# Optimization experiments

Measured on AMD Instinct MI355X. Metric: run time of the kernel, lower is better.

The kernel has to match this reference:

```python
import jax, jax.numpy as jnp
import numpy as np

HEADS = 8
GS = 16
C = 512
E = 512
SCALE = (E / HEADS) ** -0.5
PNAMES = ['sa_qkv_w','sa_qkv_b','sa_pa_w','sa_pa_b','sa_ln1_g','sa_ln1_b','sa_f1_w','sa_f1_b','sa_f2_w','sa_f2_b','sa_ln2_g','sa_ln2_b','sa_c1_w','sa_c1_b','sa_c2_w','sa_c2_b','sa_bn_g','sa_bn_b','ca_q_w','ca_q_b','ca_k_w','ca_k_b','ca_v_w','ca_v_b','ca_pa_w','ca_pa_b','p_q_w','p_q_b','p_k_w','p_k_b','p_v_w','p_v_b','p_pa_w','p_pa_b','p_ln_g','p_ln_b','p_lin_w','p_lin_b']


def _ln(x, g, b, eps=1e-5):
    m = x.mean(-1, keepdims=True)
    v = jnp.var(x, axis=-1, keepdims=True)
    return (x - m) / jnp.sqrt(v + eps) * g + b


def _conv1x1(x, w, b):
    return jnp.einsum('bchw,oc->bohw', x, w) + b[None, :, None, None]


def _up_ac(x, out=GS):
    # bilinear upsample, align_corners=True (nn.UpsamplingBilinear2d)
    H = x.shape[2]
    pos = jnp.arange(out) * (H - 1) / (out - 1)
    lo = jnp.floor(pos).astype(jnp.int32)
    hi = jnp.minimum(lo + 1, H - 1)
    w = (pos - lo).astype(x.dtype)
    xr = x[:, :, lo, :] * (1 - w)[None, None, :, None] + x[:, :, hi, :] * w[None, None, :, None]
    return xr[:, :, :, lo] * (1 - w) + xr[:, :, :, hi] * w


def _asri(x, p):
    # Sequence_ASRI: GAP tokens -> attention over the batch axis -> pixel-shuffle back
    B = x.shape[0]; ch = E // HEADS
    gap = x.mean((2, 3))                                             # [B,C]
    qkv = (gap @ p['sa_qkv_w'].T + p['sa_qkv_b']).reshape(B, 4, ch, HEADS).transpose(1, 3, 0, 2)  # [4,H,B,ch]
    q, k, v, skip = qkv[0], qkv[1], qkv[2], qkv[3]
    attn = jax.nn.softmax(jnp.einsum('hbc,hdc->hbd', q, k) * SCALE, -1)  # [H,B,B]
    o = jnp.einsum('hbd,hdc->hbc', attn, v)
    merge = lambda t: t.transpose(1, 2, 0).reshape(B, E)             # 'head b c -> b (c head)'
    a = merge(o) @ p['sa_pa_w'].T + p['sa_pa_b'] + merge(skip)
    h = jax.nn.relu(_ln(a, p['sa_ln1_g'], p['sa_ln1_b']) @ p['sa_f1_w'].T + p['sa_f1_b'])
    a = h @ p['sa_f2_w'].T + p['sa_f2_b'] + a
    s = _ln(a, p['sa_ln2_g'], p['sa_ln2_b']) @ p['sa_c1_w'].T + p['sa_c1_b']  # [B,C*16]
    s = _up_ac(s.reshape(B, C, 4, 4))                                 # pixel shuffle p1=p2=4 then bilinear to 16x16
    s = _conv1x1(s, p['sa_c2_w'], p['sa_c2_b'])
    # BatchNorm2d in eval mode (running_mean=0, running_var=1, eps=1e-5)
    s = s / np.float32(np.sqrt(1.0 + 1e-5)) * p['sa_bn_g'][None, :, None, None] + p['sa_bn_b'][None, :, None, None]
    return x + jax.nn.relu(s)


def _sscm(x1, x2, p):
    # Sequence_SSCM: GAP-token q/k over batch axis, full spatial v
    B = x1.shape[0]; ch = E // HEADS
    q = (x1.mean((2, 3)) @ p['ca_q_w'].T + p['ca_q_b']).reshape(B, ch, HEADS).transpose(2, 0, 1)  # [H,B,ch]
    k = (x2.mean((2, 3)) @ p['ca_k_w'].T + p['ca_k_b']).reshape(B, ch, HEADS).transpose(2, 0, 1)
    v = _conv1x1(x2, p['ca_v_w'], p['ca_v_b']).reshape(B, ch, HEADS, GS, GS).transpose(2, 0, 1, 3, 4).reshape(HEADS, B, ch * GS * GS)
    attn = jax.nn.softmax(jnp.einsum('hbc,hdc->hbd', q, k) * SCALE, -1)  # [H,B,B]
    o = jnp.einsum('hbd,hdm->hbm', attn, v)
    o = o.reshape(HEADS, B, ch, GS, GS).transpose(1, 2, 0, 3, 4).reshape(B, E, GS, GS)
    return jax.nn.relu(_conv1x1(o, p['ca_pa_w'], p['ca_pa_b']))


def _pixel(x1, x2, p):
    # Pixel_SSCM: pixel-wise cross-batch attention (no scale -- matches source)
    B = x1.shape[0]; ch = E // HEADS; N = GS * GS
    split = lambda t: t.reshape(B, ch, HEADS, N).transpose(2, 0, 3, 1)   # 'b (c head) h w -> head b (h w) c'
    q = split(_conv1x1(x1, p['p_q_w'], p['p_q_b']))                      # [H,B,N,ch]
    k = split(_conv1x1(x2, p['p_k_w'], p['p_k_b']))
    v = split(_conv1x1(x2, p['p_v_w'], p['p_v_b'])).reshape(HEADS, B * N, ch)
    attn = jax.nn.softmax(jnp.einsum('hbnc,hqmc->hbqnm', q, k), -1)      # [H,B,B,N,N]
    attn = attn.transpose(1, 0, 3, 2, 4).reshape(B, HEADS, N, B * N)     # 'head b q h w -> b head h (q w)'
    o = jnp.einsum('bhnm,hmc->bhnc', attn, v)
    o = o.transpose(0, 3, 1, 2).reshape(B, E, GS, GS)                    # 'b head (h w) c -> b (c head) h w'
    o = _conv1x1(o, p['p_pa_w'], p['p_pa_b']) + x1
    t = o.reshape(B, C, N).transpose(0, 2, 1)                            # [B,N,C]
    t = jax.nn.relu(_ln(t, p['p_ln_g'], p['p_ln_b']) @ p['p_lin_w'].T + p['p_lin_b'])
    return t.transpose(0, 2, 1).reshape(B, C, GS, GS)


def _hrlm(p, xs, xq):
    sa_s = _asri(xs, p)
    sa_q = _asri(xq, p)
    ca_s = _sscm(sa_s, sa_q, p)
    ca_q = _sscm(sa_q, sa_s, p)
    return _pixel(sa_s, ca_q, p), _pixel(sa_q, ca_s, p)


def setup_inputs():
    key = jax.random.key(0)
    ks = iter(jax.random.split(key, 64))
    w = lambda *s: (jax.random.normal(next(ks), s) * 0.02).astype(jnp.float32)
    z = lambda n: jnp.zeros((n,), jnp.float32)
    o = lambda n: jnp.ones((n,), jnp.float32)
    return dict(
        fea_support=jax.random.normal(next(ks), (8, C, GS, GS), jnp.float32),
        fea_query=jax.random.normal(next(ks), (8, C, GS, GS), jnp.float32),
        sa_qkv_w=w(4 * E, C), sa_qkv_b=z(4 * E),
        sa_pa_w=w(E, E), sa_pa_b=z(E),
        sa_ln1_g=o(E), sa_ln1_b=z(E),
        sa_f1_w=w(E, E), sa_f1_b=z(E), sa_f2_w=w(E, E), sa_f2_b=z(E),
        sa_ln2_g=o(E), sa_ln2_b=z(E),
        sa_c1_w=w(C * 16, E), sa_c1_b=z(C * 16),
        sa_c2_w=w(C, E), sa_c2_b=z(C),
        sa_bn_g=o(C), sa_bn_b=z(C),
        ca_q_w=w(E, C), ca_q_b=z(E), ca_k_w=w(E, C), ca_k_b=z(E),
        ca_v_w=w(E, C), ca_v_b=z(E), ca_pa_w=w(C, E), ca_pa_b=z(C),
        p_q_w=w(E, C), p_q_b=z(E), p_k_w=w(E, C), p_k_b=z(E),
        p_v_w=w(E, C), p_v_b=z(E), p_pa_w=w(C, E), p_pa_b=z(C),
        p_ln_g=o(C), p_ln_b=z(C), p_lin_w=w(C, C), p_lin_b=z(C),
    )


def reference(fea_support, fea_query, sa_qkv_w, sa_qkv_b, sa_pa_w, sa_pa_b, sa_ln1_g, sa_ln1_b, sa_f1_w, sa_f1_b, sa_f2_w, sa_f2_b, sa_ln2_g, sa_ln2_b, sa_c1_w, sa_c1_b, sa_c2_w, sa_c2_b, sa_bn_g, sa_bn_b, ca_q_w, ca_q_b, ca_k_w, ca_k_b, ca_v_w, ca_v_b, ca_pa_w, ca_pa_b, p_q_w, p_q_b, p_k_w, p_k_b, p_v_w, p_v_b, p_pa_w, p_pa_b, p_ln_g, p_ln_b, p_lin_w, p_lin_b):
    p = dict(zip(PNAMES, (sa_qkv_w, sa_qkv_b, sa_pa_w, sa_pa_b, sa_ln1_g, sa_ln1_b, sa_f1_w, sa_f1_b, sa_f2_w, sa_f2_b, sa_ln2_g, sa_ln2_b, sa_c1_w, sa_c1_b, sa_c2_w, sa_c2_b, sa_bn_g, sa_bn_b, ca_q_w, ca_q_b, ca_k_w, ca_k_b, ca_v_w, ca_v_b, ca_pa_w, ca_pa_b, p_q_w, p_q_b, p_k_w, p_k_b, p_v_w, p_v_b, p_pa_w, p_pa_b, p_ln_g, p_ln_b, p_lin_w, p_lin_b)))
    return _hrlm(p, fea_support, fea_query)
```

## Files before the change

kernel.cpp:

```cpp
#include <hip/hip_runtime.h>
#include <cmath>

#define IMG 131072
#define BIGF 1048576
#define PLANE 1048576

#define CF_RELU  1
#define CF_RES   2
#define CF_BN    4
#define CF_SPLIT 8

typedef __attribute__((ext_vector_type(8))) short short8;
typedef __attribute__((ext_vector_type(4))) short short4v;
typedef __attribute__((ext_vector_type(4))) float f32x4;

__device__ __forceinline__ float wave_sum(float v){
    #pragma unroll
    for (int off = 32; off; off >>= 1) v += __shfl_xor(v, off);
    return v;
}

__device__ __forceinline__ unsigned short bf16_rn(float x){
    union { float f; unsigned u; } v; v.f = x;
    unsigned r = v.u + 0x7FFF + ((v.u >> 16) & 1);
    return (unsigned short)(r >> 16);
}
__device__ __forceinline__ float bf16_to_f(unsigned short h){
    union { float f; unsigned u; } v; v.u = ((unsigned)h) << 16;
    return v.f;
}

struct GapJobs  { const float* x[2]; float* o[2]; };
struct G8Job    { const float* in; const float* W; const float* bias; const float* add; float* out; };
struct G8Jobs   { G8Job j[4]; };
struct AAJobs   { const float* qkv[2]; float* om[2]; };
struct LnJobs   { const float* in[2]; float* out[2]; };
struct UpJobs   { const float* in[2]; float* out[2]; };
struct SAJobs   { const float* q8[2]; const float* k8[2]; float* aw[2]; };
struct SPJobs   { const float* aw[2]; const float* v[2]; float* out[2]; };
struct ZJobs    { float* p[2]; };
struct ConvJob  { const float* X; const float* W; const float* B; const float* R;
                  const float* bng; const float* bnb; float* O; int flags; };
struct ConvJobs { ConvJob j[6]; };
struct PixJob   { const unsigned short* Q; const unsigned short* K; const unsigned short* V; float* O; };
struct PixJobs  { PixJob j[2]; };

__global__ __launch_bounds__(64) void k_gap(GapJobs jo){
    const int br = blockIdx.y;
    const int bc = blockIdx.x;
    const int lane = threadIdx.x;
    const float* p = jo.x[br] + (size_t)bc * 256;
    float s = p[lane] + p[lane + 64] + p[lane + 128] + p[lane + 192];
    s = wave_sum(s);
    if (lane == 0) jo.o[br][bc] = s * (1.0f / 256.0f);
}

__global__ __launch_bounds__(64) void k_gemm8(G8Jobs jo, int add_off, int add_stride, int O, int relu){
    const G8Job j = jo.j[blockIdx.y];
    const int o = blockIdx.x;
    const int lane = threadIdx.x;
    const float* wr = j.W + (size_t)o * 512;
    float acc[8] = {0,0,0,0,0,0,0,0};
    #pragma unroll
    for (int i = 0; i < 8; i++){
        float w = wr[lane + 64*i];
        #pragma unroll
        for (int b = 0; b < 8; b++) acc[b] += w * j.in[b*512 + lane + 64*i];
    }
    #pragma unroll
    for (int b = 0; b < 8; b++) acc[b] = wave_sum(acc[b]);
    if (lane < 8){
        float v = acc[0];
        #pragma unroll
        for (int b = 1; b < 8; b++) if (lane == b) v = acc[b];
        v += j.bias[o];
        if (j.add) v += j.add[lane*add_stride + add_off + o];
        if (relu) v = fmaxf(v, 0.f);
        j.out[(size_t)lane * O + o] = v;
    }
}

__global__ __launch_bounds__(64) void k_asri_attn(AAJobs jo){
    const int br = blockIdx.y;
    const float* qkv = jo.qkv[br];
    const int h = blockIdx.x >> 3, b = blockIdx.x & 7, c = threadIdx.x;
    const int ci = c*8 + h;
    float qc = qkv[b*2048 + ci];
    float s[8];
    #pragma unroll
    for (int d = 0; d < 8; d++){
        float p = qc * qkv[d*2048 + 512 + ci];
        p = wave_sum(p);
        s[d] = p * 0.125f;
    }
    float m = s[0];
    #pragma unroll
    for (int d = 1; d < 8; d++) m = fmaxf(m, s[d]);
    float sum = 0.f;
    #pragma unroll
    for (int d = 0; d < 8; d++){ s[d] = __expf(s[d]-m); sum += s[d]; }
    float r = 1.f / sum;
    float oc = 0.f;
    #pragma unroll
    for (int d = 0; d < 8; d++) oc += s[d]*r * qkv[d*2048 + 1024 + ci];
    jo.om[br][b*512 + ci] = oc;
}

__global__ __launch_bounds__(64) void k_ln8(LnJobs jo,
    const float* __restrict__ g, const float* __restrict__ be)
{
    const int br = blockIdx.y;
    const int b = blockIdx.x, lane = threadIdx.x;
    const float* in = jo.in[br];
    float v[8]; float s = 0.f;
    #pragma unroll
    for (int i = 0; i < 8; i++){ v[i] = in[b*512 + lane + 64*i]; s += v[i]; }
    s = wave_sum(s);
    float mean = s * (1.f/512.f);
    float q = 0.f;
    #pragma unroll
    for (int i = 0; i < 8; i++){ float d = v[i]-mean; q += d*d; }
    q = wave_sum(q);
    float rstd = rsqrtf(q*(1.f/512.f) + 1e-5f);
    #pragma unroll
    for (int i = 0; i < 8; i++){
        int c = lane + 64*i;
        jo.out[br][b*512 + c] = (v[i]-mean)*rstd*g[c] + be[c];
    }
}

__global__ __launch_bounds__(256) void k_up(UpJobs jo){
    const int br = blockIdx.y;
    const int idx = blockIdx.x*256 + threadIdx.x;
    const int x = idx & 15, y = (idx >> 4) & 15, bc = idx >> 8;
    float px = (float)(x*3) / 15.0f, py = (float)(y*3) / 15.0f;
    int lx = (int)px, ly = (int)py;
    float wx = px - lx, wy = py - ly;
    int hx = min(lx+1, 3), hy = min(ly+1, 3);
    const float* p = jo.in[br] + (size_t)bc * 16;
    float v00 = p[ly*4+lx], v01 = p[ly*4+hx], v10 = p[hy*4+lx], v11 = p[hy*4+hx];
    float a0 = v00*(1.f-wy) + v10*wy;
    float a1 = v01*(1.f-wy) + v11*wy;
    jo.out[br][idx] = a0*(1.f-wx) + a1*wx;
}

__global__ __launch_bounds__(256) void k_zero(ZJobs jo){
    jo.p[blockIdx.y][(size_t)blockIdx.x*256 + threadIdx.x] = 0.f;
}

#define LDK 40
__device__ __forceinline__ void convm_body(
    const float* __restrict__ Xb, const float* __restrict__ W,
    const float* __restrict__ bias, const float* __restrict__ resb,
    const float* __restrict__ bng, const float* __restrict__ bnb, float bninv,
    float* __restrict__ outb, int flags, int o0, int n0, unsigned short* lds)
{
    const int tid512 = threadIdx.x;
    const int g   = tid512 >> 8;
    const int tid = tid512 & 255;
    unsigned short* sAh = lds + g*10240;
    unsigned short* sAl = sAh + 2560;
    unsigned short* sBh = sAl + 2560;
    unsigned short* sBl = sBh + 2560;
    const int wv = tid >> 6, lane = tid & 63;
    const int quad = lane >> 4, l16 = lane & 15;
    const int wo = (wv >> 1) * 32, wn = (wv & 1) * 32;
    const int so  = tid >> 2, sk8 = (tid & 3) * 8;
    const int sp  = tid & 15, sn  = (tid >> 4) * 4;

    const float* wrow = W + (size_t)(o0 + so)*512 + g*256 + sk8;
    const float* xrow = Xb + (size_t)(g*256 + 2*sp)*256 + n0 + sn;

    f32x4 acc[2][2] = {};
    float4 a0 = *(const float4*)(wrow);
    float4 a1 = *(const float4*)(wrow + 4);
    float4 x0 = *(const float4*)(xrow);
    float4 x1 = *(const float4*)(xrow + 256);

    for (int k0 = 0; k0 < 256; k0 += 32){
        __syncthreads();
        {
            float wa[8] = {a0.x,a0.y,a0.z,a0.w,a1.x,a1.y,a1.z,a1.w};
            #pragma unroll
            for (int j = 0; j < 4; j++){
                unsigned short h0 = bf16_rn(wa[2*j]);
                unsigned short h1 = bf16_rn(wa[2*j+1]);
                unsigned short g0 = bf16_rn(wa[2*j]   - bf16_to_f(h0));
                unsigned short g1 = bf16_rn(wa[2*j+1] - bf16_to_f(h1));
                *(unsigned*)&sAh[so*LDK + sk8 + 2*j] = (unsigned)h0 | ((unsigned)h1 << 16);
                *(unsigned*)&sAl[so*LDK + sk8 + 2*j] = (unsigned)g0 | ((unsigned)g1 << 16);
            }
            float xe[4] = {x0.x,x0.y,x0.z,x0.w};
            float xo[4] = {x1.x,x1.y,x1.z,x1.w};
            #pragma unroll
            for (int j = 0; j < 4; j++){
                unsigned short h0 = bf16_rn(xe[j]);
                unsigned short h1 = bf16_rn(xo[j]);
                unsigned short g0 = bf16_rn(xe[j] - bf16_to_f(h0));
                unsigned short g1 = bf16_rn(xo[j] - bf16_to_f(h1));
                *(unsigned*)&sBh[(sn+j)*LDK + 2*sp] = (unsigned)h0 | ((unsigned)h1 << 16);
                *(unsigned*)&sBl[(sn+j)*LDK + 2*sp] = (unsigned)g0 | ((unsigned)g1 << 16);
            }
        }
        __syncthreads();
        if (k0 + 32 < 256){
            a0 = *(const float4*)(wrow + k0 + 32);
            a1 = *(const float4*)(wrow + k0 + 36);
            x0 = *(const float4*)(xrow + (size_t)(k0+32)*256);
            x1 = *(const float4*)(xrow + (size_t)(k0+32)*256 + 256);
        }
        short8 ah[2], al[2], bh[2], bl[2];
        #pragma unroll
        for (int t = 0; t < 2; t++){
            int ai = (wo + 16*t + l16)*LDK + quad*8;
            ah[t] = *(const short8*)&sAh[ai];
            al[t] = *(const short8*)&sAl[ai];
            int bi = (wn + 16*t + l16)*LDK + quad*8;
            bh[t] = *(const short8*)&sBh[bi];
            bl[t] = *(const short8*)&sBl[bi];
        }
        #pragma unroll
        for (int mt = 0; mt < 2; mt++){
            #pragma unroll
            for (int nt = 0; nt < 2; nt++){
                acc[mt][nt] = __builtin_amdgcn_mfma_f32_16x16x32_bf16(ah[mt], bh[nt], acc[mt][nt], 0, 0, 0);
                acc[mt][nt] = __builtin_amdgcn_mfma_f32_16x16x32_bf16(ah[mt], bl[nt], acc[mt][nt], 0, 0, 0);
                acc[mt][nt] = __builtin_amdgcn_mfma_f32_16x16x32_bf16(al[mt], bh[nt], acc[mt][nt], 0, 0, 0);
            }
        }
    }
    __syncthreads();
    float* red = (float*)lds;
    if (g == 1){
        float* r = red + tid*20;
        #pragma unroll
        for (int mt = 0; mt < 2; mt++)
            #pragma unroll
            for (int nt = 0; nt < 2; nt++)
                *(f32x4*)(r + (mt*2+nt)*4) = acc[mt][nt];
    }
    __syncthreads();
    if (g == 0){
        float* r = red + tid*20;
        #pragma unroll
        for (int mt = 0; mt < 2; mt++)
            #pragma unroll
            for (int nt = 0; nt < 2; nt++){
                f32x4 o4 = *(const f32x4*)(r + (mt*2+nt)*4);
                acc[mt][nt] += o4;
            }
        #pragma unroll
        for (int mt = 0; mt < 2; mt++){
            #pragma unroll
            for (int nt = 0; nt < 2; nt++){
                const int n  = n0 + wn + 16*nt + l16;
                const int ob = o0 + wo + 16*mt + quad*4;
                #pragma unroll
                for (int rr = 0; rr < 4; rr++){
                    const int o = ob + rr;
                    float v = acc[mt][nt][rr] + bias[o];
                    if (flags & CF_BN)   v = v*(bninv*bng[o]) + bnb[o];
                    if (flags & CF_RELU) v = fmaxf(v, 0.f);
                    if (flags & CF_RES)  v += resb[(size_t)o*256 + n];
                    if (flags & CF_SPLIT){
                        unsigned short hi = bf16_rn(v);
                        unsigned short lo = bf16_rn(v - bf16_to_f(hi));
                        unsigned short* oh = (unsigned short*)outb;
                        oh[(size_t)o*256 + n] = hi;
                        oh[PLANE + (size_t)o*256 + n] = lo;
                    } else {
                        outb[(size_t)o*256 + n] = v;
                    }
                }
            }
        }
    }
}

__global__ __launch_bounds__(512) void k_convm(ConvJobs jo, float bninv)
{
    __shared__ unsigned short lds[20480];
    const int z = blockIdx.z;
    const ConvJob j = jo.j[z >> 3];
    const int b = z & 7;
    float* ob = (j.flags & CF_SPLIT) ? j.O + (size_t)b*(IMG/2) : j.O + (size_t)b*IMG;
    convm_body(j.X + (size_t)b*IMG, j.W, j.B, j.R ? j.R + (size_t)b*IMG : nullptr,
               j.bng, j.bnb, bninv, ob, j.flags,
               blockIdx.y*64, blockIdx.x*64, lds);
}

__global__ __launch_bounds__(64) void k_sscm_attn(SAJobs jo)
{
    const int br = blockIdx.y;
    const int h = blockIdx.x >> 3, b = blockIdx.x & 7, c = threadIdx.x;
    const int ci = c*8 + h;
    float qc = jo.q8[br][b*512 + ci];
    float s[8];
    #pragma unroll
    for (int d = 0; d < 8; d++){
        float p = qc * jo.k8[br][d*512 + ci];
        p = wave_sum(p);
        s[d] = p * 0.125f;
    }
    float m = s[0];
    #pragma unroll
    for (int d = 1; d < 8; d++) m = fmaxf(m, s[d]);
    float sum = 0.f;
    #pragma unroll
    for (int d = 0; d < 8; d++){ s[d] = __expf(s[d]-m); sum += s[d]; }
    float r = 1.f/sum;
    if (c < 8){
        float v = s[0];
        #pragma unroll
        for (int d = 1; d < 8; d++) if (c == d) v = s[d];
        jo.aw[br][blockIdx.x*8 + c] = v*r;
    }
}

__global__ __launch_bounds__(256) void k_sscm_apply(SPJobs jo)
{
    const int br = blockIdx.y;
    const int idx = blockIdx.x*256 + threadIdx.x;
    const int pix = idx & 255, e = (idx >> 8) & 511, b = idx >> 17;
    const int h = e & 7;
    const float* aw = jo.aw[br] + (h*8 + b)*8;
    const float* v = jo.v[br];
    float acc = 0.f;
    #pragma unroll
    for (int d = 0; d < 8; d++) acc += aw[d] * v[(size_t)d*IMG + (size_t)e*256 + pix];
    jo.out[br][idx] = acc;
}

__global__ __launch_bounds__(256) void k_pixel_mfma(PixJobs jo)
{
    __shared__ char smem[61440];
    unsigned short* sQh = (unsigned short*)smem;
    unsigned short* sQl = sQh + 2*64*40;
    unsigned short* sKh = sQl + 2*64*40;
    unsigned short* sKl = sKh + 2*128*40;
    unsigned short* sP  = (unsigned short*)smem;
    unsigned short* sVh = sP  + 4*64*40;
    unsigned short* sVl = sVh + 4*64*40;

    const int br = blockIdx.y >> 3, b = blockIdx.y & 7;
    const PixJob J = jo.j[br];
    const int nt = blockIdx.x & 3, d = blockIdx.x >> 2;
    const int h = blockIdx.z;
    const int tid = threadIdx.x;
    const int wv = tid >> 6, lane = tid & 63;
    const int quad = lane >> 4, l16 = lane & 15;
    const int n0 = nt * 64;

    const unsigned short* Qh = J.Q + (size_t)b * 131072;
    const unsigned short* Ql = Qh + PLANE;
    const unsigned short* Kh = J.K + (size_t)d * 131072;
    const unsigned short* Kl = Kh + PLANE;
    const unsigned short* Vh = J.V + (size_t)d * 131072;
    const unsigned short* Vl = Vh + PLANE;

    {
        const int q = tid & 63, c0 = tid >> 6;
        #pragma unroll
        for (int r = 0; r < 16; r++){
            int c = c0 + 4*r;
            int src = (c*8+h)*256 + n0 + q;
            int idx = (c>>5)*2560 + q*40 + (c&31);
            sQh[idx] = Qh[src];
            sQl[idx] = Ql[src];
        }
    }
    __syncthreads();

    short8 bqh[2], bql[2];
    #pragma unroll
    for (int ks = 0; ks < 2; ks++){
        int idx = ks*2560 + (wv*16 + l16)*40 + quad*8;
        bqh[ks] = *(const short8*)&sQh[idx];
        bql[ks] = *(const short8*)&sQl[idx];
    }

    f32x4 S[16] = {};
    #pragma unroll
    for (int hm = 0; hm < 2; hm++){
        __syncthreads();
        {
            const int mloc = tid & 127, cb0 = tid >> 7;
            #pragma unroll
            for (int p = 0; p < 4; p++){
                int cb = cb0 + 2*p;
                short8 hi8, lo8;
                #pragma unroll
                for (int j = 0; j < 8; j++){
                    int src = ((cb*8+j)*8+h)*256 + hm*128 + mloc;
                    hi8[j] = (short)Kh[src];
                    lo8[j] = (short)Kl[src];
                }
                int idx = (cb>>2)*5120 + mloc*40 + (cb&3)*8;
                *(short8*)&sKh[idx] = hi8;
                *(short8*)&sKl[idx] = lo8;
            }
        }
        __syncthreads();
        #pragma unroll
        for (int mtl = 0; mtl < 8; mtl++){
            #pragma unroll
            for (int ks = 0; ks < 2; ks++){
                int idx = ks*5120 + (mtl*16 + l16)*40 + quad*8;
                short8 ah = *(const short8*)&sKh[idx];
                short8 al = *(const short8*)&sKl[idx];
                S[hm*8+mtl] = __builtin_amdgcn_mfma_f32_16x16x32_bf16(ah, bqh[ks], S[hm*8+mtl], 0, 0, 0);
                S[hm*8+mtl] = __builtin_amdgcn_mfma_f32_16x16x32_bf16(ah, bql[ks], S[hm*8+mtl], 0, 0, 0);
                S[hm*8+mtl] = __builtin_amdgcn_mfma_f32_16x16x32_bf16(al, bqh[ks], S[hm*8+mtl], 0, 0, 0);
            }
        }
    }

    {
        float mx = -3.4e38f;
        #pragma unroll
        for (int t = 0; t < 16; t++)
            #pragma unroll
            for (int r = 0; r < 4; r++) mx = fmaxf(mx, S[t][r]);
        mx = fmaxf(mx, __shfl_xor(mx, 16));
        mx = fmaxf(mx, __shfl_xor(mx, 32));
        float sum = 0.f;
        #pragma unroll
        for (int t = 0; t < 16; t++)
            #pragma unroll
            for (int r = 0; r < 4; r++){ S[t][r] = __expf(S[t][r]-mx); sum += S[t][r]; }
        sum += __shfl_xor(sum, 16);
        sum += __shfl_xor(sum, 32);
        float rr = 1.f/sum;
        #pragma unroll
        for (int t = 0; t < 16; t++)
            #pragma unroll
            for (int r = 0; r < 4; r++) S[t][r] *= rr;
    }

    f32x4 oac[4] = {};
    #pragma unroll
    for (int hm = 0; hm < 2; hm++){
        __syncthreads();
        #pragma unroll
        for (int mtl = 0; mtl < 8; mtl++){
            short4v p4;
            #pragma unroll
            for (int r = 0; r < 4; r++) p4[r] = (short)bf16_rn(S[hm*8+mtl][r]);
            int idx = (mtl>>1)*2560 + (wv*16 + l16)*40 + 16*(mtl&1) + quad*4;
            *(short4v*)&sP[idx] = p4;
        }
        {
            const int mp = tid & 63, c0 = tid >> 6;
            #pragma unroll
            for (int p = 0; p < 16; p++){
                int c = c0 + 4*p;
                int src = (c*8+h)*256 + hm*128 + 2*mp;
                int idx = (mp>>4)*2560 + c*40 + ((2*mp)&31);
                *(unsigned*)&sVh[idx] = *(const unsigned*)&Vh[src];
                *(unsigned*)&sVl[idx] = *(const unsigned*)&Vl[src];
            }
        }
        __syncthreads();
        #pragma unroll
        for (int ks = 0; ks < 4; ks++){
            int pidx = ks*2560 + (wv*16 + l16)*40 + quad*8;
            short8 bp = *(const short8*)&sP[pidx];
            #pragma unroll
            for (int ct = 0; ct < 4; ct++){
                int vidx = ks*2560 + (ct*16 + l16)*40 + quad*8;
                short8 vh = *(const short8*)&sVh[vidx];
                short8 vl = *(const short8*)&sVl[vidx];
                oac[ct] = __builtin_amdgcn_mfma_f32_16x16x32_bf16(vh, bp, oac[ct], 0, 0, 0);
                oac[ct] = __builtin_amdgcn_mfma_f32_16x16x32_bf16(vl, bp, oac[ct], 0, 0, 0);
            }
        }
    }

    {
        float* Ob = J.O + (size_t)b * IMG;
        const int q = n0 + wv*16 + l16;
        #pragma unroll
        for (int ct = 0; ct < 4; ct++){
            #pragma unroll
            for (int r = 0; r < 4; r++){
                int c = ct*16 + quad*4 + r;
                unsafeAtomicAdd(&Ob[(size_t)(c*8+h)*256 + q], oac[ct][r]);
            }
        }
    }
}

__global__ __launch_bounds__(64) void k_ln_pix(LnJobs jo,
    const float* __restrict__ g, const float* __restrict__ be)
{
    const int br = blockIdx.y;
    const int bn = blockIdx.x;
    const int b = bn >> 8, n = bn & 255;
    const int lane = threadIdx.x;
    const float* p = jo.in[br] + (size_t)b*IMG + n;
    float v[8]; float s = 0.f;
    #pragma unroll
    for (int i = 0; i < 8; i++){ v[i] = p[(size_t)(lane + 64*i)*256]; s += v[i]; }
    s = wave_sum(s);
    float mean = s * (1.f/512.f);
    float q = 0.f;
    #pragma unroll
    for (int i = 0; i < 8; i++){ float d = v[i]-mean; q += d*d; }
    q = wave_sum(q);
    float rstd = rsqrtf(q*(1.f/512.f) + 1e-5f);
    #pragma unroll
    for (int i = 0; i < 8; i++){
        int c = lane + 64*i;
        jo.out[br][(size_t)b*IMG + (size_t)c*256 + n] = (v[i]-mean)*rstd*g[c] + be[c];
    }
}

extern "C" void kernel_launch(void* const* d_in, const int* in_sizes, int n_in,
                              void* d_out, int out_size, void* d_ws, size_t ws_size,
                              hipStream_t stream)
{
    const float* xs    = (const float*)d_in[0];
    const float* xq    = (const float*)d_in[1];
    const float* qkvw  = (const float*)d_in[2];  const float* qkvb = (const float*)d_in[3];
    const float* paw   = (const float*)d_in[4];  const float* pab  = (const float*)d_in[5];
    const float* ln1g  = (const float*)d_in[6];  const float* ln1b = (const float*)d_in[7];
    const float* f1w   = (const float*)d_in[8];  const float* f1b  = (const float*)d_in[9];
    const float* f2w   = (const float*)d_in[10]; const float* f2b  = (const float*)d_in[11];
    const float* ln2g  = (const float*)d_in[12]; const float* ln2b = (const float*)d_in[13];
    const float* c1w   = (const float*)d_in[14]; const float* c1b  = (const float*)d_in[15];
    const float* c2w   = (const float*)d_in[16]; const float* c2b  = (const float*)d_in[17];
    const float* bng   = (const float*)d_in[18]; const float* bnb  = (const float*)d_in[19];
    const float* caqw  = (const float*)d_in[20]; const float* caqb = (const float*)d_in[21];
    const float* cakw  = (const float*)d_in[22]; const float* cakb = (const float*)d_in[23];
    const float* cavw  = (const float*)d_in[24]; const float* cavb = (const float*)d_in[25];
    const float* capw  = (const float*)d_in[26]; const float* capb = (const float*)d_in[27];
    const float* pqw   = (const float*)d_in[28]; const float* pqb  = (const float*)d_in[29];
    const float* pkw   = (const float*)d_in[30]; const float* pkb  = (const float*)d_in[31];
    const float* pvw   = (const float*)d_in[32]; const float* pvb  = (const float*)d_in[33];
    const float* ppw   = (const float*)d_in[34]; const float* ppb  = (const float*)d_in[35];
    const float* plng  = (const float*)d_in[36]; const float* plnb = (const float*)d_in[37];
    const float* plinw = (const float*)d_in[38]; const float* plinb= (const float*)d_in[39];

    const size_t SMF = 262144;
    float* ws = (float*)d_ws;
    float* smb = ws;
    float* B[12];
    for (int i = 0; i < 12; i++) B[i] = ws + SMF + (size_t)i*BIGF;
    float* sa_s = B[0]; float* sa_q = B[1];
    float* ca_s = B[2]; float* ca_q = B[3];
    const bool paired_pixel = ws_size >= (SMF + 12*(size_t)BIGF)*sizeof(float) + 1024;

    auto SM = [&](int br){ return smb + (size_t)br*131072; };
    auto GAP=[&](int br){ return SM(br); };            auto QKV=[&](int br){ return SM(br)+4096; };
    auto OM =[&](int br){ return SM(br)+20480; };      auto AA =[&](int br){ return SM(br)+24576; };
    auto HB =[&](int br){ return SM(br)+28672; };      auto A2 =[&](int br){ return SM(br)+32768; };
    auto LNB=[&](int br){ return SM(br)+36864; };      auto S8 =[&](int br){ return SM(br)+40960; };
    auto ATW=[&](int br){ return SM(br)+106496; };     auto Q8 =[&](int br){ return SM(br)+107008; };
    auto K8 =[&](int br){ return SM(br)+111104; };

    const float bninv = 1.0f / sqrtf(1.0f + 1e-5f);
    float* out0 = (float*)d_out;
    float* out1 = out0 + (size_t)BIGF;

    {
        GapJobs gj = {{xs, xq}, {GAP(0), GAP(1)}};
        k_gap<<<dim3(4096,2), 64, 0, stream>>>(gj);
        G8Jobs qj = {{{GAP(0), qkvw, qkvb, nullptr, QKV(0)}, {GAP(1), qkvw, qkvb, nullptr, QKV(1)}}};
        k_gemm8<<<dim3(2048,2), 64, 0, stream>>>(qj, 0, 0, 2048, 0);
        AAJobs aj = {{QKV(0), QKV(1)}, {OM(0), OM(1)}};
        k_asri_attn<<<dim3(64,2), 64, 0, stream>>>(aj);
        G8Jobs pj = {{{OM(0), paw, pab, QKV(0), AA(0)}, {OM(1), paw, pab, QKV(1), AA(1)}}};
        k_gemm8<<<dim3(512,2), 64, 0, stream>>>(pj, 1536, 2048, 512, 0);
        LnJobs l1 = {{AA(0), AA(1)}, {LNB(0), LNB(1)}};
        k_ln8<<<dim3(8,2), 64, 0, stream>>>(l1, ln1g, ln1b);
        G8Jobs fj = {{{LNB(0), f1w, f1b, nullptr, HB(0)}, {LNB(1), f1w, f1b, nullptr, HB(1)}}};
        k_gemm8<<<dim3(512,2), 64, 0, stream>>>(fj, 0, 0, 512, 1);
        G8Jobs f2j = {{{HB(0), f2w, f2b, AA(0), A2(0)}, {HB(1), f2w, f2b, AA(1), A2(1)}}};
        k_gemm8<<<dim3(512,2), 64, 0, stream>>>(f2j, 0, 512, 512, 0);
        LnJobs l2 = {{A2(0), A2(1)}, {LNB(0), LNB(1)}};
        k_ln8<<<dim3(8,2), 64, 0, stream>>>(l2, ln2g, ln2b);
        G8Jobs cj = {{{LNB(0), c1w, c1b, nullptr, S8(0)}, {LNB(1), c1w, c1b, nullptr, S8(1)}}};
        k_gemm8<<<dim3(8192,2), 64, 0, stream>>>(cj, 0, 0, 8192, 0);
        UpJobs uj = {{S8(0), S8(1)}, {B[4], B[5]}};
        k_up<<<dim3(4096,2), 256, 0, stream>>>(uj);
        ConvJobs c2j = {};
        c2j.j[0] = {B[4], c2w, c2b, xs, bng, bnb, sa_s, CF_BN|CF_RELU|CF_RES};
        c2j.j[1] = {B[5], c2w, c2b, xq, bng, bnb, sa_q, CF_BN|CF_RELU|CF_RES};
        k_convm<<<dim3(4,8,16), 512, 0, stream>>>(c2j, bninv);
    }

    {
        GapJobs gj = {{sa_s, sa_q}, {GAP(0), GAP(1)}};
        k_gap<<<dim3(4096,2), 64, 0, stream>>>(gj);
        G8Jobs qj = {{{GAP(0), caqw, caqb, nullptr, Q8(0)},
                      {GAP(1), cakw, cakb, nullptr, K8(0)},
                      {GAP(1), caqw, caqb, nullptr, Q8(1)},
                      {GAP(0), cakw, cakb, nullptr, K8(1)}}};
        k_gemm8<<<dim3(512,4), 64, 0, stream>>>(qj, 0, 0, 512, 0);
        SAJobs sj = {{Q8(0), Q8(1)}, {K8(0), K8(1)}, {ATW(0), ATW(1)}};
        k_sscm_attn<<<dim3(64,2), 64, 0, stream>>>(sj);
        ConvJobs vj = {};
        vj.j[0] = {sa_q, cavw, cavb, nullptr, nullptr, nullptr, B[4], 0};
        vj.j[1] = {sa_s, cavw, cavb, nullptr, nullptr, nullptr, B[5], 0};
        k_convm<<<dim3(4,8,16), 512, 0, stream>>>(vj, 1.f);
        SPJobs pj = {{ATW(0), ATW(1)}, {B[4], B[5]}, {B[6], B[7]}};
        k_sscm_apply<<<dim3(4096,2), 256, 0, stream>>>(pj);
        ConvJobs aj = {};
        aj.j[0] = {B[6], capw, capb, nullptr, nullptr, nullptr, ca_s, CF_RELU};
        aj.j[1] = {B[7], capw, capb, nullptr, nullptr, nullptr, ca_q, CF_RELU};
        k_convm<<<dim3(4,8,16), 512, 0, stream>>>(aj, 1.f);
    }

    if (paired_pixel){
        ConvJobs qkvj = {};
        qkvj.j[0] = {sa_s, pqw, pqb, nullptr, nullptr, nullptr, B[4],  CF_SPLIT};
        qkvj.j[1] = {ca_q, pkw, pkb, nullptr, nullptr, nullptr, B[5],  CF_SPLIT};
        qkvj.j[2] = {ca_q, pvw, pvb, nullptr, nullptr, nullptr, B[6],  CF_SPLIT};
        qkvj.j[3] = {sa_q, pqw, pqb, nullptr, nullptr, nullptr, B[8],  CF_SPLIT};
        qkvj.j[4] = {ca_s, pkw, pkb, nullptr, nullptr, nullptr, B[9],  CF_SPLIT};
        qkvj.j[5] = {ca_s, pvw, pvb, nullptr, nullptr, nullptr, B[10], CF_SPLIT};
        k_convm<<<dim3(4,8,48), 512, 0, stream>>>(qkvj, 1.f);
        ZJobs zj = {{B[7], B[11]}};
        k_zero<<<dim3(4096,2), 256, 0, stream>>>(zj);
        PixJobs pxj = {{{(const unsigned short*)B[4], (const unsigned short*)B[5], (const unsigned short*)B[6], B[7]},
                        {(const unsigned short*)B[8], (const unsigned short*)B[9], (const unsigned short*)B[10], B[11]}}};
        k_pixel_mfma<<<dim3(32,16,8), 256, 0, stream>>>(pxj);
        ConvJobs ppj = {};
        ppj.j[0] = {B[7],  ppw, ppb, sa_s, nullptr, nullptr, out0, CF_RES};
        ppj.j[1] = {B[11], ppw, ppb, sa_q, nullptr, nullptr, out1, CF_RES};
        k_convm<<<dim3(4,8,16), 512, 0, stream>>>(ppj, 1.f);
        LnJobs lj = {{out0, out1}, {B[4], B[8]}};
        k_ln_pix<<<dim3(2048,2), 64, 0, stream>>>(lj, plng, plnb);
        ConvJobs lnj = {};
        lnj.j[0] = {B[4], plinw, plinb, nullptr, nullptr, nullptr, out0, CF_RELU};
        lnj.j[1] = {B[8], plinw, plinb, nullptr, nullptr, nullptr, out1, CF_RELU};
        k_convm<<<dim3(4,8,16), 512, 0, stream>>>(lnj, 1.f);
    } else {
        auto pixel1 = [&](const float* x1, const float* x2, float* out){
            ConvJobs qkvj = {};
            qkvj.j[0] = {x1, pqw, pqb, nullptr, nullptr, nullptr, B[4], CF_SPLIT};
            qkvj.j[1] = {x2, pkw, pkb, nullptr, nullptr, nullptr, B[5], CF_SPLIT};
            qkvj.j[2] = {x2, pvw, pvb, nullptr, nullptr, nullptr, B[6], CF_SPLIT};
            k_convm<<<dim3(4,8,24), 512, 0, stream>>>(qkvj, 1.f);
            ZJobs zj = {{B[7], B[7]}};
            k_zero<<<dim3(4096,1), 256, 0, stream>>>(zj);
            PixJobs pxj = {{{(const unsigned short*)B[4], (const unsigned short*)B[5], (const unsigned short*)B[6], B[7]},
                            {(const unsigned short*)B[4], (const unsigned short*)B[5], (const unsigned short*)B[6], B[7]}}};
            k_pixel_mfma<<<dim3(32,8,8), 256, 0, stream>>>(pxj);
            ConvJobs ppj = {};
            ppj.j[0] = {B[7], ppw, ppb, x1, nullptr, nullptr, out, CF_RES};
            k_convm<<<dim3(4,8,8), 512, 0, stream>>>(ppj, 1.f);
            LnJobs lj = {{out, out}, {B[4], B[4]}};
            k_ln_pix<<<dim3(2048,1), 64, 0, stream>>>(lj, plng, plnb);
            ConvJobs lnj = {};
            lnj.j[0] = {B[4], plinw, plinb, nullptr, nullptr, nullptr, out, CF_RELU};
            k_convm<<<dim3(4,8,8), 512, 0, stream>>>(lnj, 1.f);
        };
        pixel1(sa_s, ca_q, out0);
        pixel1(sa_q, ca_s, out1);
    }

    (void)in_sizes; (void)n_in; (void)out_size;
}
```

Baseline: 579.3 us.

## Interleave hi/lo bf16 split planes and transpose Q/K for vectorized pixel-attention loads

The QKV 1x1 conv now packs the hi and lo bf16 halves of each value into one 32-bit word instead of writing two separate planes. For Q and K it also writes a transposed, head-grouped layout (pixel-major, then head, then channel). The pixel attention kernel can then stage Q and K tiles with 16-byte vector loads and split hi/lo with byte permutes, replacing strided per-element 2-byte gathers. The transposed epilogue stores are scattered with a 2 KB stride, which may cost write efficiency in the conv kernel.

```diff
diff --git a/kernel.cpp b/kernel.cpp
--- a/kernel.cpp
+++ b/kernel.cpp
@@ -3,12 +3,12 @@
 
 #define IMG 131072
 #define BIGF 1048576
-#define PLANE 1048576
 
 #define CF_RELU  1
 #define CF_RES   2
 #define CF_BN    4
 #define CF_SPLIT 8
+#define CF_TRANS 16
 
 typedef __attribute__((ext_vector_type(8))) short short8;
 typedef __attribute__((ext_vector_type(4))) short short4v;
@@ -28,6 +28,12 @@
 __device__ __forceinline__ float bf16_to_f(unsigned short h){
     union { float f; unsigned u; } v; v.u = ((unsigned)h) << 16;
     return v.f;
+}
+__device__ __forceinline__ unsigned pk_hi(unsigned a, unsigned b){
+    return __builtin_amdgcn_perm(b, a, 0x05040100u);
+}
+__device__ __forceinline__ unsigned pk_lo(unsigned a, unsigned b){
+    return __builtin_amdgcn_perm(b, a, 0x07060302u);
 }
 
 struct GapJobs  { const float* x[2]; float* o[2]; };
@@ -42,7 +48,7 @@
 struct ConvJob  { const float* X; const float* W; const float* B; const float* R;
                   const float* bng; const float* bnb; float* O; int flags; };
 struct ConvJobs { ConvJob j[6]; };
-struct PixJob   { const unsigned short* Q; const unsigned short* K; const unsigned short* V; float* O; };
+struct PixJob   { const unsigned* Q; const unsigned* K; const unsigned* V; float* O; };
 struct PixJobs  { PixJob j[2]; };
 
 __global__ __launch_bounds__(64) void k_gap(GapJobs jo){
@@ -265,9 +271,10 @@
                     if (flags & CF_SPLIT){
                         unsigned short hi = bf16_rn(v);
                         unsigned short lo = bf16_rn(v - bf16_to_f(hi));
-                        unsigned short* oh = (unsigned short*)outb;
-                        oh[(size_t)o*256 + n] = hi;
-                        oh[PLANE + (size_t)o*256 + n] = lo;
+                        unsigned pk = (unsigned)hi | ((unsigned)lo << 16);
+                        unsigned* op = (unsigned*)outb;
+                        if (flags & CF_TRANS) op[(size_t)n*512 + (o&7)*64 + (o>>3)] = pk;
+                        else                  op[(size_t)o*256 + n] = pk;
                     } else {
                         outb[(size_t)o*256 + n] = v;
                     }
@@ -283,9 +290,8 @@
     const int z = blockIdx.z;
     const ConvJob j = jo.j[z >> 3];
     const int b = z & 7;
-    float* ob = (j.flags & CF_SPLIT) ? j.O + (size_t)b*(IMG/2) : j.O + (size_t)b*IMG;
     convm_body(j.X + (size_t)b*IMG, j.W, j.B, j.R ? j.R + (size_t)b*IMG : nullptr,
-               j.bng, j.bnb, bninv, ob, j.flags,
+               j.bng, j.bnb, bninv, j.O + (size_t)b*IMG, j.flags,
                blockIdx.y*64, blockIdx.x*64, lds);
 }
 
@@ -351,23 +357,24 @@
     const int quad = lane >> 4, l16 = lane & 15;
     const int n0 = nt * 64;
 
-    const unsigned short* Qh = J.Q + (size_t)b * 131072;
-    const unsigned short* Ql = Qh + PLANE;
-    const unsigned short* Kh = J.K + (size_t)d * 131072;
-    const unsigned short* Kl = Kh + PLANE;
-    const unsigned short* Vh = J.V + (size_t)d * 131072;
-    const unsigned short* Vl = Vh + PLANE;
-
     {
-        const int q = tid & 63, c0 = tid >> 6;
-        #pragma unroll
-        for (int r = 0; r < 16; r++){
-            int c = c0 + 4*r;
-            int src = (c*8+h)*256 + n0 + q;
-            int idx = (c>>5)*2560 + q*40 + (c&31);
-            sQh[idx] = Qh[src];
-            sQl[idx] = Ql[src];
-        }
+        const unsigned* Qt = J.Q + (size_t)b*IMG + (size_t)n0*512 + h*64;
+        const int q = tid >> 2, i0 = (tid & 3) * 16;
+        const unsigned* src = Qt + (size_t)q*512 + i0;
+        uint4 w0 = *(const uint4*)(src);
+        uint4 w1 = *(const uint4*)(src + 4);
+        uint4 w2 = *(const uint4*)(src + 8);
+        uint4 w3 = *(const uint4*)(src + 12);
+        unsigned hb[8], lb[8];
+        hb[0]=pk_hi(w0.x,w0.y); hb[1]=pk_hi(w0.z,w0.w); hb[2]=pk_hi(w1.x,w1.y); hb[3]=pk_hi(w1.z,w1.w);
+        hb[4]=pk_hi(w2.x,w2.y); hb[5]=pk_hi(w2.z,w2.w); hb[6]=pk_hi(w3.x,w3.y); hb[7]=pk_hi(w3.z,w3.w);
+        lb[0]=pk_lo(w0.x,w0.y); lb[1]=pk_lo(w0.z,w0.w); lb[2]=pk_lo(w1.x,w1.y); lb[3]=pk_lo(w1.z,w1.w);
+        lb[4]=pk_lo(w2.x,w2.y); lb[5]=pk_lo(w2.z,w2.w); lb[6]=pk_lo(w3.x,w3.y); lb[7]=pk_lo(w3.z,w3.w);
+        int dst = (i0>>5)*2560 + q*40 + (i0&31);
+        *(uint4*)&sQh[dst]     = *(uint4*)&hb[0];
+        *(uint4*)&sQh[dst + 8] = *(uint4*)&hb[4];
+        *(uint4*)&sQl[dst]     = *(uint4*)&lb[0];
+        *(uint4*)&sQl[dst + 8] = *(uint4*)&lb[4];
     }
     __syncthreads();
 
@@ -384,20 +391,22 @@
     for (int hm = 0; hm < 2; hm++){
         __syncthreads();
         {
+            const unsigned* Kt = J.K + (size_t)d*IMG + (size_t)hm*128*512 + h*64;
             const int mloc = tid & 127, cb0 = tid >> 7;
             #pragma unroll
             for (int p = 0; p < 4; p++){
                 int cb = cb0 + 2*p;
-                short8 hi8, lo8;
-                #pragma unroll
-                for (int j = 0; j < 8; j++){
-                    int src = ((cb*8+j)*8+h)*256 + hm*128 + mloc;
-                    hi8[j] = (short)Kh[src];
-                    lo8[j] = (short)Kl[src];
-                }
+                const unsigned* src = Kt + (size_t)mloc*512 + cb*8;
+                uint4 wa = *(const uint4*)(src);
+                uint4 wb = *(const uint4*)(src + 4);
+                union { short8 s; unsigned u[4]; } hu, lu;
+                hu.u[0]=pk_hi(wa.x,wa.y); hu.u[1]=pk_hi(wa.z,wa.w);
+                hu.u[2]=pk_hi(wb.x,wb.y); hu.u[3]=pk_hi(wb.z,wb.w);
+                lu.u[0]=pk_lo(wa.x,wa.y); lu.u[1]=pk_lo(wa.z,wa.w);
+                lu.u[2]=pk_lo(wb.x,wb.y); lu.u[3]=pk_lo(wb.z,wb.w);
                 int idx = (cb>>2)*5120 + mloc*40 + (cb&3)*8;
-                *(short8*)&sKh[idx] = hi8;
-                *(short8*)&sKl[idx] = lo8;
+                *(short8*)&sKh[idx] = hu.s;
+                *(short8*)&sKl[idx] = lu.s;
             }
         }
         __syncthreads();
@@ -450,14 +459,16 @@
             *(short4v*)&sP[idx] = p4;
         }
         {
+            const unsigned* Vp = J.V + (size_t)d*IMG + (size_t)h*256 + hm*128;
             const int mp = tid & 63, c0 = tid >> 6;
             #pragma unroll
             for (int p = 0; p < 16; p++){
                 int c = c0 + 4*p;
-                int src = (c*8+h)*256 + hm*128 + 2*mp;
+                const unsigned* src = Vp + (size_t)c*2048 + 2*mp;
+                uint2 w = *(const uint2*)(src);
                 int idx = (mp>>4)*2560 + c*40 + ((2*mp)&31);
-                *(unsigned*)&sVh[idx] = *(const unsigned*)&Vh[src];
-                *(unsigned*)&sVl[idx] = *(const unsigned*)&Vl[src];
+                *(unsigned*)&sVh[idx] = pk_hi(w.x, w.y);
+                *(unsigned*)&sVl[idx] = pk_lo(w.x, w.y);
             }
         }
         __syncthreads();
@@ -613,17 +624,17 @@
 
     if (paired_pixel){
         ConvJobs qkvj = {};
-        qkvj.j[0] = {sa_s, pqw, pqb, nullptr, nullptr, nullptr, B[4],  CF_SPLIT};
-        qkvj.j[1] = {ca_q, pkw, pkb, nullptr, nullptr, nullptr, B[5],  CF_SPLIT};
+        qkvj.j[0] = {sa_s, pqw, pqb, nullptr, nullptr, nullptr, B[4],  CF_SPLIT|CF_TRANS};
+        qkvj.j[1] = {ca_q, pkw, pkb, nullptr, nullptr, nullptr, B[5],  CF_SPLIT|CF_TRANS};
         qkvj.j[2] = {ca_q, pvw, pvb, nullptr, nullptr, nullptr, B[6],  CF_SPLIT};
-        qkvj.j[3] = {sa_q, pqw, pqb, nullptr, nullptr, nullptr, B[8],  CF_SPLIT};
-        qkvj.j[4] = {ca_s, pkw, pkb, nullptr, nullptr, nullptr, B[9],  CF_SPLIT};
+        qkvj.j[3] = {sa_q, pqw, pqb, nullptr, nullptr, nullptr, B[8],  CF_SPLIT|CF_TRANS};
+        qkvj.j[4] = {ca_s, pkw, pkb, nullptr, nullptr, nullptr, B[9],  CF_SPLIT|CF_TRANS};
         qkvj.j[5] = {ca_s, pvw, pvb, nullptr, nullptr, nullptr, B[10], CF_SPLIT};
         k_convm<<<dim3(4,8,48), 512, 0, stream>>>(qkvj, 1.f);
         ZJobs zj = {{B[7], B[11]}};
         k_zero<<<dim3(4096,2), 256, 0, stream>>>(zj);
-        PixJobs pxj = {{{(const unsigned short*)B[4], (const unsigned short*)B[5], (const unsigned short*)B[6], B[7]},
-                        {(const unsigned short*)B[8], (const unsigned short*)B[9], (const unsigned short*)B[10], B[11]}}};
+        PixJobs pxj = {{{(const unsigned*)B[4], (const unsigned*)B[5], (const unsigned*)B[6], B[7]},
+                        {(const unsigned*)B[8], (const unsigned*)B[9], (const unsigned*)B[10], B[11]}}};
         k_pixel_mfma<<<dim3(32,16,8), 256, 0, stream>>>(pxj);
         ConvJobs ppj = {};
         ppj.j[0] = {B[7],  ppw, ppb, sa_s, nullptr, nullptr, out0, CF_RES};
@@ -638,14 +649,14 @@
     } else {
         auto pixel1 = [&](const float* x1, const float* x2, float* out){
             ConvJobs qkvj = {};
-            qkvj.j[0] = {x1, pqw, pqb, nullptr, nullptr, nullptr, B[4], CF_SPLIT};
-            qkvj.j[1] = {x2, pkw, pkb, nullptr, nullptr, nullptr, B[5], CF_SPLIT};
+            qkvj.j[0] = {x1, pqw, pqb, nullptr, nullptr, nullptr, B[4], CF_SPLIT|CF_TRANS};
+            qkvj.j[1] = {x2, pkw, pkb, nullptr, nullptr, nullptr, B[5], CF_SPLIT|CF_TRANS};
             qkvj.j[2] = {x2, pvw, pvb, nullptr, nullptr, nullptr, B[6], CF_SPLIT};
             k_convm<<<dim3(4,8,24), 512, 0, stream>>>(qkvj, 1.f);
             ZJobs zj = {{B[7], B[7]}};
             k_zero<<<dim3(4096,1), 256, 0, stream>>>(zj);
-            PixJobs pxj = {{{(const unsigned short*)B[4], (const unsigned short*)B[5], (const unsigned short*)B[6], B[7]},
-                            {(const unsigned short*)B[4], (const unsigned short*)B[5], (const unsigned short*)B[6], B[7]}}};
+            PixJobs pxj = {{{(const unsigned*)B[4], (const unsigned*)B[5], (const unsigned*)B[6], B[7]},
+                            {(const unsigned*)B[4], (const unsigned*)B[5], (const unsigned*)B[6], B[7]}}};
             k_pixel_mfma<<<dim3(32,8,8), 256, 0, stream>>>(pxj);
             ConvJobs ppj = {};
             ppj.j[0] = {B[7], ppw, ppb, x1, nullptr, nullptr, out, CF_RES};
```

Result: faster. 492.6 us (-15.0%).
